# Performance work log

Hardware: AMD Instinct MI355X
Metric: run time of the kernel (lower is better)

## Reference

```python
import jax, jax.numpy as jnp
import numpy as np

EPS_NORM = 1e-12   # torch F.normalize eps
GN_EPS = 1e-5      # GroupNorm eps
FACTOR = 5
NUM_HEADS = 8
NEG_SLOPE = 0.01   # LeakyReLU default


def _l2norm(x, axis):
    n = jnp.sqrt(jnp.sum(x * x, axis=axis, keepdims=True))
    return x / jnp.maximum(n, EPS_NORM)


def setup_inputs() -> dict:
    key = jax.random.key(0)
    B, C, H, W, D = 2, 256, 16, 16, 16
    N = H * W * D
    sample_k = FACTOR * int(np.ceil(np.log(N)))  # 45
    ks = jax.random.split(key, 8)
    s = 0.02
    return {
        "x": jax.random.normal(ks[0], (B, C, H, W, D), jnp.float32),
        "W_qkvv": jax.random.normal(ks[1], (C, 4 * C), jnp.float32) * s,
        "W_out": jax.random.normal(ks[2], (C, C), jnp.float32) * s,
        "b_out": jnp.zeros((C,), jnp.float32),
        "W_out2": jax.random.normal(ks[3], (C, C), jnp.float32) * s,
        "b_out2": jnp.zeros((C,), jnp.float32),
        "gamma1": 0.1 * jnp.ones((C,), jnp.float32),
        "conv_w": jax.random.normal(ks[4], (C, C, 3, 3, 3), jnp.float32) * s,
        "gn_w": jnp.ones((C,), jnp.float32),
        "gn_b": jnp.zeros((C,), jnp.float32),
        "index_sample": jax.random.randint(ks[5], (N, sample_k), 0, N),
    }


def reference(x, W_qkvv, W_out, b_out, W_out2, b_out2, gamma1, conv_w, gn_w, gn_b, index_sample):
    B, C, H, Wd, D = x.shape
    N = H * Wd * D
    nh = NUM_HEADS
    dh = C // nh
    xs = x.reshape(B, C, N).transpose(0, 2, 1)                    # [B,N,C]
    qkvv = (xs @ W_qkvv).reshape(B, N, 4, nh, dh).transpose(2, 0, 3, 1, 4)  # [4,B,nh,N,dh]
    q, k, v_ca, v_sa = qkvv[0], qkvv[1], qkvv[2], qkvv[3]
    q = _l2norm(q, axis=-2)   # normalize over sequence dim (dim=-2 in torch)
    k = _l2norm(k, axis=-2)

    u = FACTOR * int(np.ceil(np.log(N)))
    # --- ProbSparse _prob_QK ---
    K_sample = k[:, :, index_sample, :]                            # [B,nh,N,sk,dh]
    QK_sample = jnp.einsum('bhle,bhlse->bhls', q, K_sample)        # [B,nh,N,sk]
    M = QK_sample.max(-1) - QK_sample.sum(-1) / N                  # sparsity measure
    _, M_top = jax.lax.top_k(M, u)                                 # [B,nh,u]
    b_idx = jnp.arange(B)[:, None, None]
    h_idx = jnp.arange(nh)[None, :, None]
    Q_red = q[b_idx, h_idx, M_top]                                 # [B,nh,u,dh]
    scores = jnp.einsum('bhud,bhld->bhul', Q_red, k)               # [B,nh,u,N]

    # --- spatial (ProbSparse) context ---
    ctx = jnp.broadcast_to(v_sa.mean(axis=-2, keepdims=True), v_sa.shape)  # [B,nh,N,dh]
    attn_sa = jax.nn.softmax(scores, axis=-1)
    upd = jnp.einsum('bhul,bhld->bhud', attn_sa, v_sa)             # [B,nh,u,dh]
    ctx = ctx.at[b_idx, h_idx, M_top].set(upd)

    # --- channel attention (on transposed q,k,v: [B,nh,dh,N]) ---
    qt = q.transpose(0, 1, 3, 2)
    kt = k.transpose(0, 1, 3, 2)
    vt = v_ca.transpose(0, 1, 3, 2)
    attn_ca = jax.nn.softmax(jnp.einsum('bhdn,bhen->bhde', qt, kt), axis=-1)  # [B,nh,dh,dh]
    x_ca = jnp.einsum('bhde,bhen->bhdn', attn_ca, vt).transpose(0, 3, 1, 2).reshape(B, N, C)
    x_sa = ctx.transpose(0, 3, 1, 2).reshape(B, N, C)              # matches source permute
    x_sa = x_sa @ W_out + b_out                                    # dead branch (source discards)
    x_ca = x_ca @ W_out2 + b_out2
    epa = x_ca  # source: x = x_SA + x_CA; x = x_CA  -> only CA branch survives

    attn = xs + gamma1 * epa                                       # [B,N,C]
    attn = attn.reshape(B, H, Wd, D, C).transpose(0, 4, 1, 2, 3)   # [B,C,H,W,D]

    # conv8: Dropout3d (eval=id) -> Conv3d(3x3x3, no bias) -> GroupNorm(1 group)
    y = jax.lax.conv_general_dilated(attn, conv_w, (1, 1, 1), [(1, 1)] * 3,
                                     dimension_numbers=('NCDHW', 'OIDHW', 'NCDHW'))
    mu = y.mean(axis=(1, 2, 3, 4), keepdims=True)
    var = y.var(axis=(1, 2, 3, 4), keepdims=True)
    y = (y - mu) / jnp.sqrt(var + GN_EPS)
    y = y * gn_w[None, :, None, None, None] + gn_b[None, :, None, None, None]
    y = y + attn
    return jnp.where(y >= 0, y, NEG_SLOPE * y)
```

## Files before the change

### kernel.cpp

```cpp
#include <hip/hip_runtime.h>
#include <hip/hip_bf16.h>
#include <stdint.h>


#define B_ 2
#define C_ 256
#define N_ 4096
#define NH 8
#define PADV 5832
#define CN  (C_*N_)
#define BCN (B_*CN)

typedef unsigned short u16;
typedef unsigned int   u32;

using frag16 = __attribute__((ext_vector_type(8))) short;
using f32x4  = __attribute__((ext_vector_type(4))) float;

__device__ __forceinline__ u16 f2bf(float f) {
    u32 u = __float_as_uint(f);
    u += 0x7fff + ((u >> 16) & 1);
    return (u16)(u >> 16);
}
__device__ __forceinline__ float bb(u16 h) { return __uint_as_float((u32)h << 16); }
__device__ __forceinline__ void gld16(const void* g, void* l) {
    __builtin_amdgcn_global_load_lds((const __attribute__((address_space(1))) u32*)g,
                                     (__attribute__((address_space(3))) u32*)l, 16, 0, 0);
}
__device__ __forceinline__ int padrow(int n) {
    int z = n >> 8, y = (n >> 4) & 15, x = n & 15;
    return (z + 1) * 324 + (y + 1) * 18 + (x + 1);
}

#define OFF_XB16  0
#define OFF_GP    1048576
#define OFF_NQK   2097152
#define OFF_PK    0
#define OFF_Y     3145728
#define OFF_ATTB  4194304
#define OFF_ATTP  5242880
#define OFF_WT2   6735872
#define OFF_W2B   7620608
#define OFF_WQB   7653376
#define OFF_XT    7751680
#define OFF_WVT   8800256
#define OFF_BD    8833024
#define OFF_MT    8898560
#define OFF_WFU   8964096
#define OFF_NRM   9029632
#define OFF_RED   9030656

__global__ __launch_bounds__(256) void k_prep(const float* __restrict__ CW, const float* __restrict__ W2,
                                              const float* __restrict__ Wq, const float* __restrict__ X,
                                              u16* __restrict__ WT2, u16* __restrict__ W2B,
                                              u16* __restrict__ Wqb, u16* __restrict__ WvT,
                                              u16* __restrict__ XT, u16* __restrict__ XB,
                                              u32* __restrict__ APz, float* __restrict__ NRM) {
    __shared__ __align__(16) float ls[6912];
    float (*ts)[33] = (float(*)[33])ls;
    float (*t64)[65] = (float(*)[65])ls;
    int blk = blockIdx.x, tid = threadIdx.x;
    if (blk < 256) {
        int co = blk;
        const float* src = CW + (size_t)co * 6912;
        for (int u = tid; u < 6912; u += 256) ls[u] = src[u];
        __syncthreads();
#pragma unroll
        for (int t = 0; t < 27; ++t)
            WT2[(((size_t)t * 256 + co) << 8) + tid] = f2bf(ls[tid * 27 + t]);
    } else if (blk < 320) {
        int bi = blk - 256; int c0 = (bi & 7) * 32, p0 = (bi >> 3) * 32;
        int tx = tid & 31, ty = tid >> 5;
#pragma unroll
        for (int i = 0; i < 4; ++i) ts[ty + i * 8][tx] = W2[(size_t)(p0 + ty + i * 8) * 256 + c0 + tx];
        __syncthreads();
#pragma unroll
        for (int i = 0; i < 4; ++i) W2B[(size_t)(c0 + ty + i * 8) * 256 + p0 + tx] = f2bf(ts[tx][ty + i * 8]);
    } else if (blk < 512) {
        int bi = blk - 320; int c0 = (bi & 7) * 32, j0 = (bi >> 3) * 32;
        int tx = tid & 31, ty = tid >> 5;
#pragma unroll
        for (int i = 0; i < 4; ++i) ts[ty + i * 8][tx] = Wq[(size_t)(c0 + ty + i * 8) * 1024 + j0 + tx];
        __syncthreads();
#pragma unroll
        for (int i = 0; i < 4; ++i) Wqb[(size_t)(j0 + ty + i * 8) * 256 + c0 + tx] = f2bf(ts[tx][ty + i * 8]);
    } else if (blk < 768) {
        int c = blk - 512;
        WvT[(size_t)c * 256 + tid] = f2bf(Wq[(size_t)c * 1024 + 512 + tid]);
    } else if (blk < 1280) {
        int idx = blk - 768;
        int n0 = (idx & 63) * 64, c0 = ((idx >> 6) & 3) * 64, b = idx >> 8;
        int tn = tid & 63, tc4 = tid >> 6;
        const float* Xb = X + (size_t)b * CN;
        u16* XBb = XB + (size_t)b * CN;
#pragma unroll
        for (int i = 0; i < 16; ++i) {
            int c = c0 + tc4 + i * 4;
            float v = Xb[(size_t)c * N_ + n0 + tn];
            t64[tc4 + i * 4][tn] = v;
            XBb[(size_t)c * N_ + n0 + tn] = f2bf(v);
        }
        __syncthreads();
        u16* Xo = XT + (size_t)b * N_ * C_;
#pragma unroll
        for (int i = 0; i < 16; ++i)
            Xo[(size_t)(n0 + tc4 + i * 4) * C_ + c0 + tn] = f2bf(t64[tn][tc4 + i * 4]);
    } else if (blk < 7112) {
        APz[(size_t)(blk - 1280) * 256 + tid] = 0;
    } else {
        ((float4*)NRM)[tid] = make_float4(0.f, 0.f, 0.f, 0.f);
    }
}

__global__ __launch_bounds__(256) void k_gram(const u16* __restrict__ XB, float* __restrict__ GP) {
    __shared__ __align__(16) u16 As[2][8192], Bs[2][8192];
    int mt = blockIdx.x & 1, nt = blockIdx.x >> 1, s = blockIdx.y, b = blockIdx.z;
    int c0 = mt * 128, c0p = nt * 128, k0 = s * 512;
    int tid = threadIdx.x, lane = tid & 63, w = tid >> 6;
    int wm = w & 1, wn = w >> 1, qm = lane >> 4, lm = lane & 15;
    int srow = lane >> 3;
    int sperm = (((lane & 7) ^ srow) << 3);
    const u16* aB = XB + ((size_t)(b * 256 + c0 + w * 32 + srow)) * 4096 + k0 + sperm;
    const u16* bB = XB + ((size_t)(b * 256 + c0p + w * 32 + srow)) * 4096 + k0 + sperm;
    int rdp = ((lm & 7) << 3);
    f32x4 acc[4][4] = {};
    auto stg = [&](int p, int kt) {
#pragma unroll
        for (int i = 0; i < 4; ++i) {
            gld16(aB + (size_t)i * 32768 + kt * 64, &As[p][w * 2048 + i * 512]);
            gld16(bB + (size_t)i * 32768 + kt * 64, &Bs[p][w * 2048 + i * 512]);
        }
    };
    stg(0, 0);
#pragma unroll
    for (int kt = 0; kt < 8; ++kt) {
        int p = kt & 1;
        __syncthreads();
        if (kt < 7) stg(p ^ 1, kt + 1);
#pragma unroll
        for (int c2 = 0; c2 < 2; ++c2) {
            frag16 af[4], bf[4];
#pragma unroll
            for (int i = 0; i < 4; ++i)
                af[i] = *(const frag16*)&As[p][(wm * 64 + i * 16 + lm) * 64 + ((((c2 * 4 + qm) << 3) ^ rdp))];
#pragma unroll
            for (int j = 0; j < 4; ++j)
                bf[j] = *(const frag16*)&Bs[p][(wn * 64 + j * 16 + lm) * 64 + ((((c2 * 4 + qm) << 3) ^ rdp))];
#pragma unroll
            for (int i = 0; i < 4; ++i)
#pragma unroll
                for (int j = 0; j < 4; ++j)
                    acc[i][j] = __builtin_amdgcn_mfma_f32_16x16x32_bf16(af[i], bf[j], acc[i][j], 0, 0, 0);
        }
    }
    float* o = GP + (((size_t)s * B_ + b) * 256 + c0 + wm * 64) * 256 + c0p + wn * 64;
#pragma unroll
    for (int i = 0; i < 4; ++i)
#pragma unroll
        for (int j = 0; j < 4; ++j)
#pragma unroll
            for (int r = 0; r < 4; ++r)
                o[(size_t)(i * 16 + qm * 4 + r) * 256 + j * 16 + lm] = acc[i][j][r];
}

__global__ __launch_bounds__(256) void k_nqk(const float* __restrict__ GP, const u16* __restrict__ Wqb,
                                             u16* __restrict__ NQK, float* __restrict__ NRM) {
    __shared__ float Gs[16][260];
    int ct = blockIdx.x, h = blockIdx.y, b = blockIdx.z, t = threadIdx.x;
#pragma unroll
    for (int i = 0; i < 16; ++i) {
        float v = 0.f;
#pragma unroll
        for (int s = 0; s < 8; ++s)
            v += GP[(((size_t)s * B_ + b) * 256 + ct * 16 + i) * 256 + t];
        Gs[i][t] = v;
    }
    __syncthreads();
    int o = t >> 3, cg = t & 7;
    int cl0 = cg * 2, cl1 = cg * 2 + 1;
    const u16* Wk = Wqb + (size_t)(256 + h * 32 + o) * 256;
    const u16* Wqr = Wqb + (size_t)(h * 32 + o) * 256;
    float ak0 = 0.f, ak1 = 0.f, aq0 = 0.f, aq1 = 0.f;
    for (int cp = 0; cp < 256; cp += 8) {
        uint4 kv = *(const uint4*)(Wk + cp);
        uint4 qv = *(const uint4*)(Wqr + cp);
        const u16 *kh = (const u16*)&kv, *qh = (const u16*)&qv;
#pragma unroll
        for (int j = 0; j < 8; ++j) {
            float kf = bb(kh[j]), qf = bb(qh[j]);
            float g0 = Gs[cl0][cp + j], g1v = Gs[cl1][cp + j];
            ak0 += kf * g0; ak1 += kf * g1v;
            aq0 += qf * g0; aq1 += qf * g1v;
        }
    }
    size_t base_q = (((size_t)(b * NH + h) * 2 + 0) * 32 + o) * 256 + ct * 16 + cg * 2;
    *(u32*)(NQK + base_q)        = (u32)f2bf(aq0) | ((u32)f2bf(aq1) << 16);
    *(u32*)(NQK + base_q + 8192) = (u32)f2bf(ak0) | ((u32)f2bf(ak1) << 16);
    u32 wq = *(const u32*)(Wqr + ct * 16 + cg * 2);
    u32 wk = *(const u32*)(Wk + ct * 16 + cg * 2);
    float pq = bb((u16)wq) * aq0 + bb((u16)(wq >> 16)) * aq1;
    float pk = bb((u16)wk) * ak0 + bb((u16)(wk >> 16)) * ak1;
    pq += __shfl_xor(pq, 1); pq += __shfl_xor(pq, 2); pq += __shfl_xor(pq, 4);
    pk += __shfl_xor(pk, 1); pk += __shfl_xor(pk, 2); pk += __shfl_xor(pk, 4);
    if (cg == 0) {
        atomicAdd(&NRM[b * 512 + h * 64 + o], pq);
        atomicAdd(&NRM[b * 512 + h * 64 + 32 + o], pk);
    }
}

__global__ __launch_bounds__(256) void k_soft(const u16* __restrict__ NQK, const u16* __restrict__ Wqb,
                                              const float* __restrict__ NRM, u16* __restrict__ BD) {
    __shared__ __align__(16) u16 Ws[8192], Ns[8192];
    __shared__ float Sm[32][33];
    __shared__ float Ab[32][33];
    __shared__ float iqS[32], ikS[32];
    int h = blockIdx.x, b = blockIdx.y;
    int tid = threadIdx.x, lane = tid & 63, w = tid >> 6;
    int wm = w & 1, wn = w >> 1, qm = lane >> 4, lm = lane & 15;
    const u16* Wq = Wqb + ((size_t)h * 32) * 256;
    const u16* NK = NQK + (((size_t)(b * NH + h) * 2 + 1) * 32) * 256;
#pragma unroll
    for (int rp = 0; rp < 4; ++rp) {
        int row = rp * 8 + w * 2 + (lane >> 5);
        int cg = (lane & 31) ^ (row & 31);
        gld16(Wq + (size_t)row * 256 + cg * 8, &Ws[rp * 2048 + w * 512]);
        gld16(NK + (size_t)row * 256 + cg * 8, &Ns[rp * 2048 + w * 512]);
    }
    if (tid < 32) {
        iqS[tid] = 1.0f / fmaxf(sqrtf(fmaxf(NRM[b * 512 + h * 64 + tid], 0.f)), 1e-12f);
        ikS[tid] = 1.0f / fmaxf(sqrtf(fmaxf(NRM[b * 512 + h * 64 + 32 + tid], 0.f)), 1e-12f);
    }
    __syncthreads();
    f32x4 acc = {};
    int rowA = wm * 16 + lm, rowB = wn * 16 + lm;
#pragma unroll
    for (int kk = 0; kk < 8; ++kk) {
        int sA = ((kk * 4 + qm) ^ (rowA & 31)) << 3;
        int sB = ((kk * 4 + qm) ^ (rowB & 31)) << 3;
        frag16 af = *(const frag16*)&Ws[rowA * 256 + sA];
        frag16 bf = *(const frag16*)&Ns[rowB * 256 + sB];
        acc = __builtin_amdgcn_mfma_f32_16x16x32_bf16(af, bf, acc, 0, 0, 0);
    }
#pragma unroll
    for (int r = 0; r < 4; ++r) Sm[wm * 16 + qm * 4 + r][wn * 16 + lm] = acc[r];
    __syncthreads();
    if (tid < 32) {
        float iq = iqS[tid];
        float sv[32], m = -1e30f;
#pragma unroll
        for (int e = 0; e < 32; ++e) { sv[e] = Sm[tid][e] * iq * ikS[e]; m = fmaxf(m, sv[e]); }
        float sm = 0.f;
#pragma unroll
        for (int e = 0; e < 32; ++e) { sv[e] = __expf(sv[e] - m); sm += sv[e]; }
        float rin = 1.0f / sm;
#pragma unroll
        for (int e = 0; e < 32; ++e) Ab[tid][e] = sv[e] * rin;
    }
    __syncthreads();
    u16* Bo = BD + ((size_t)b * 256 + h * 32) * 256 + tid;
    bool own = (tid >> 5) == h;
    int e = tid & 31;
#pragma unroll
    for (int d = 0; d < 32; ++d)
        Bo[(size_t)d * 256] = own ? f2bf(Ab[d][e]) : (u16)0;
}

__global__ __launch_bounds__(256) void k_mt(const u16* __restrict__ WvT, const u16* __restrict__ BD,
                                            u16* __restrict__ MT) {
    __shared__ __align__(16) u16 As[2][8192], Bs[2][8192];
    int c0 = blockIdx.x * 128, j0 = blockIdx.y * 128, b = blockIdx.z;
    int tid = threadIdx.x, lane = tid & 63, w = tid >> 6;
    int wm = w & 1, wn = w >> 1, qm = lane >> 4, lm = lane & 15;
    int srow = lane >> 3;
    int sperm = (((lane & 7) ^ srow) << 3);
    const u16* aB = WvT + ((size_t)(c0 + w * 32 + srow)) * 256 + sperm;
    const u16* bB = BD + ((size_t)(b * 256 + j0 + w * 32 + srow)) * 256 + sperm;
    int rdp = ((lm & 7) << 3);
    f32x4 acc[4][4] = {};
    auto stg = [&](int p, int kc) {
#pragma unroll
        for (int i = 0; i < 4; ++i) {
            gld16(aB + i * 2048 + kc * 64, &As[p][w * 2048 + i * 512]);
            gld16(bB + i * 2048 + kc * 64, &Bs[p][w * 2048 + i * 512]);
        }
    };
    stg(0, 0);
#pragma unroll
    for (int kt = 0; kt < 4; ++kt) {
        int p = kt & 1;
        __syncthreads();
        if (kt < 3) stg(p ^ 1, kt + 1);
#pragma unroll
        for (int c2 = 0; c2 < 2; ++c2) {
            frag16 af[4], bf[4];
#pragma unroll
            for (int i = 0; i < 4; ++i)
                af[i] = *(const frag16*)&As[p][(wm * 64 + i * 16 + lm) * 64 + ((((c2 * 4 + qm) << 3) ^ rdp))];
#pragma unroll
            for (int j = 0; j < 4; ++j)
                bf[j] = *(const frag16*)&Bs[p][(wn * 64 + j * 16 + lm) * 64 + ((((c2 * 4 + qm) << 3) ^ rdp))];
#pragma unroll
            for (int i = 0; i < 4; ++i)
#pragma unroll
                for (int j = 0; j < 4; ++j)
                    acc[i][j] = __builtin_amdgcn_mfma_f32_16x16x32_bf16(af[i], bf[j], acc[i][j], 0, 0, 0);
        }
    }
#pragma unroll
    for (int i = 0; i < 4; ++i)
#pragma unroll
        for (int r = 0; r < 4; ++r) {
            int c = c0 + wm * 64 + i * 16 + qm * 4 + r;
#pragma unroll
            for (int j = 0; j < 4; ++j)
                MT[((size_t)b * 256 + c) * 256 + j0 + wn * 64 + j * 16 + lm] = f2bf(acc[i][j][r]);
        }
}

__global__ __launch_bounds__(256) void k_wfull(const u16* __restrict__ W2B, const u16* __restrict__ MT,
                                               const float* __restrict__ g1, u16* __restrict__ WFU) {
    __shared__ __align__(16) u16 As[2][8192], Bs[2][8192];
    int c0 = blockIdx.x * 128, cq0 = blockIdx.y * 128, b = blockIdx.z;
    int tid = threadIdx.x, lane = tid & 63, w = tid >> 6;
    int wm = w & 1, wn = w >> 1, qm = lane >> 4, lm = lane & 15;
    int srow = lane >> 3;
    int sperm = (((lane & 7) ^ srow) << 3);
    const u16* aB = W2B + ((size_t)(c0 + w * 32 + srow)) * 256 + sperm;
    const u16* bB = MT + ((size_t)(b * 256 + cq0 + w * 32 + srow)) * 256 + sperm;
    int rdp = ((lm & 7) << 3);
    f32x4 acc[4][4] = {};
    auto stg = [&](int p, int kc) {
#pragma unroll
        for (int i = 0; i < 4; ++i) {
            gld16(aB + i * 2048 + kc * 64, &As[p][w * 2048 + i * 512]);
            gld16(bB + i * 2048 + kc * 64, &Bs[p][w * 2048 + i * 512]);
        }
    };
    stg(0, 0);
#pragma unroll
    for (int kt = 0; kt < 4; ++kt) {
        int p = kt & 1;
        __syncthreads();
        if (kt < 3) stg(p ^ 1, kt + 1);
#pragma unroll
        for (int c2 = 0; c2 < 2; ++c2) {
            frag16 af[4], bf[4];
#pragma unroll
            for (int i = 0; i < 4; ++i)
                af[i] = *(const frag16*)&As[p][(wm * 64 + i * 16 + lm) * 64 + ((((c2 * 4 + qm) << 3) ^ rdp))];
#pragma unroll
            for (int j = 0; j < 4; ++j)
                bf[j] = *(const frag16*)&Bs[p][(wn * 64 + j * 16 + lm) * 64 + ((((c2 * 4 + qm) << 3) ^ rdp))];
#pragma unroll
            for (int i = 0; i < 4; ++i)
#pragma unroll
                for (int j = 0; j < 4; ++j)
                    acc[i][j] = __builtin_amdgcn_mfma_f32_16x16x32_bf16(af[i], bf[j], acc[i][j], 0, 0, 0);
        }
    }
#pragma unroll
    for (int i = 0; i < 4; ++i)
#pragma unroll
        for (int r = 0; r < 4; ++r) {
            int c = c0 + wm * 64 + i * 16 + qm * 4 + r;
            float gv = g1[c];
#pragma unroll
            for (int j = 0; j < 4; ++j) {
                int cc = cq0 + wn * 64 + j * 16 + lm;
                WFU[((size_t)b * 256 + c) * 256 + cc] = f2bf(gv * acc[i][j][r]);
            }
        }
}

__global__ __launch_bounds__(256) void k_att(const u16* __restrict__ WFU, const u16* __restrict__ XT,
                                             const float* __restrict__ bias2, const float* __restrict__ g1,
                                             const float* __restrict__ X, u16* __restrict__ ATTb,
                                             u16* __restrict__ ATTp) {
    __shared__ __align__(16) u16 As[2][8192], Bs[2][8192];
    int n0 = blockIdx.x * 128, c0 = blockIdx.y * 128, b = blockIdx.z;
    int tid = threadIdx.x, lane = tid & 63, w = tid >> 6;
    int wm = w & 1, wn = w >> 1, qm = lane >> 4, lm = lane & 15;
    int srow = lane >> 3;
    int sperm = (((lane & 7) ^ srow) << 3);
    const u16* aB = WFU + ((size_t)(b * 256 + c0 + w * 32 + srow)) * 256 + sperm;
    const u16* bB = XT + ((size_t)(b * N_ + n0 + w * 32 + srow)) * 256 + sperm;
    int rdp = ((lm & 7) << 3);
    f32x4 acc[4][4] = {};
    auto stg = [&](int p, int kc) {
#pragma unroll
        for (int i = 0; i < 4; ++i) {
            gld16(aB + i * 2048 + kc * 64, &As[p][w * 2048 + i * 512]);
            gld16(bB + i * 2048 + kc * 64, &Bs[p][w * 2048 + i * 512]);
        }
    };
    stg(0, 0);
#pragma unroll
    for (int kt = 0; kt < 4; ++kt) {
        int p = kt & 1;
        __syncthreads();
        if (kt < 3) stg(p ^ 1, kt + 1);
#pragma unroll
        for (int c2 = 0; c2 < 2; ++c2) {
            frag16 af[4], bf[4];
#pragma unroll
            for (int i = 0; i < 4; ++i)
                af[i] = *(const frag16*)&As[p][(wm * 64 + i * 16 + lm) * 64 + ((((c2 * 4 + qm) << 3) ^ rdp))];
#pragma unroll
            for (int j = 0; j < 4; ++j)
                bf[j] = *(const frag16*)&Bs[p][(wn * 64 + j * 16 + lm) * 64 + ((((c2 * 4 + qm) << 3) ^ rdp))];
#pragma unroll
            for (int i = 0; i < 4; ++i)
#pragma unroll
                for (int j = 0; j < 4; ++j)
                    acc[i][j] = __builtin_amdgcn_mfma_f32_16x16x32_bf16(af[i], bf[j], acc[i][j], 0, 0, 0);
        }
    }
    int c_base = c0 + wm * 64, n_base = n0 + wn * 64;
    const float* xin = X + (size_t)b * CN;
    u16* Ao = ATTb + (size_t)b * CN;
    u16* Ap = ATTp + ((size_t)b * PADV << 8);
    float val[4][4][4];
#pragma unroll
    for (int i = 0; i < 4; ++i)
#pragma unroll
        for (int r = 0; r < 4; ++r) {
            int c = c_base + i * 16 + qm * 4 + r;
            float gb2 = g1[c] * bias2[c];
#pragma unroll
            for (int j = 0; j < 4; ++j) {
                int n = n_base + j * 16 + lm;
                float v = xin[(size_t)c * N_ + n] + acc[i][j][r] + gb2;
                val[i][j][r] = v;
                Ao[(size_t)c * N_ + n] = f2bf(v);
            }
        }
#pragma unroll
    for (int j = 0; j < 4; ++j) {
        int n = n_base + j * 16 + lm;
        int pr = padrow(n);
#pragma unroll
        for (int i = 0; i < 4; ++i) {
            ushort4 pk;
            pk.x = f2bf(val[i][j][0]); pk.y = f2bf(val[i][j][1]);
            pk.z = f2bf(val[i][j][2]); pk.w = f2bf(val[i][j][3]);
            *(ushort4*)&Ap[((size_t)pr << 8) + c_base + i * 16 + qm * 4] = pk;
        }
    }
}

__global__ __launch_bounds__(256) void k_conv_mfma(const u16* __restrict__ WT2, const u16* __restrict__ ATTp,
                                                   u16* __restrict__ Pk) {
    __shared__ __align__(16) u16 As[2][8192], Bs[2][8192];
    int n0 = blockIdx.x * 128;
    int co0 = (blockIdx.y & 1) * 128, ks = blockIdx.y >> 1;
    int b = blockIdx.z;
    int tid = threadIdx.x, lane = tid & 63, w = tid >> 6;
    int wm = w & 1, wn = w >> 1, qm = lane >> 4, lm = lane & 15;
    int srow = lane >> 3;
    int sperm = (((lane & 7) ^ srow) << 3);
    const u16* aB = WT2 + (((size_t)ks * 9 * 256 + co0 + w * 32 + srow) << 8) + sperm;
    int prA[4];
#pragma unroll
    for (int i = 0; i < 4; ++i) prA[i] = padrow(n0 + w * 32 + i * 8 + srow) << 8;
    const u16* bB = ATTp + ((size_t)b * PADV << 8) + ((ks - 1) * 324 << 8) + sperm;
    int rdp = ((lm & 7) << 3);
    f32x4 acc[4][4] = {};
    auto stg = [&](int p, int kt) {
        int tap9 = kt >> 2, kc = kt & 3;
        int K9 = ((tap9 / 3) - 1) * 18 + (tap9 % 3 - 1);
#pragma unroll
        for (int i = 0; i < 4; ++i) {
            gld16(aB + (size_t)tap9 * 65536 + i * 2048 + kc * 64, &As[p][w * 2048 + i * 512]);
            gld16(bB + prA[i] + K9 * 256 + kc * 64,              &Bs[p][w * 2048 + i * 512]);
        }
    };
    stg(0, 0);
#pragma unroll
    for (int kt = 0; kt < 36; ++kt) {
        int p = kt & 1;
        __syncthreads();
        if (kt < 35) stg(p ^ 1, kt + 1);
#pragma unroll
        for (int c2 = 0; c2 < 2; ++c2) {
            frag16 af[4], bf[4];
#pragma unroll
            for (int i = 0; i < 4; ++i)
                af[i] = *(const frag16*)&As[p][(wm * 64 + i * 16 + lm) * 64 + ((((c2 * 4 + qm) << 3) ^ rdp))];
#pragma unroll
            for (int j = 0; j < 4; ++j)
                bf[j] = *(const frag16*)&Bs[p][(wn * 64 + j * 16 + lm) * 64 + ((((c2 * 4 + qm) << 3) ^ rdp))];
#pragma unroll
            for (int i = 0; i < 4; ++i)
#pragma unroll
                for (int j = 0; j < 4; ++j)
                    acc[i][j] = __builtin_amdgcn_mfma_f32_16x16x32_bf16(af[i], bf[j], acc[i][j], 0, 0, 0);
        }
    }
    u16* Pb = Pk + ((size_t)(ks * B_ + b) * C_ + co0 + wm * 64) * N_ + n0 + wn * 64;
#pragma unroll
    for (int i = 0; i < 4; ++i)
#pragma unroll
        for (int j = 0; j < 4; ++j)
#pragma unroll
            for (int r = 0; r < 4; ++r)
                Pb[(size_t)(i * 16 + qm * 4 + r) * N_ + j * 16 + lm] = f2bf(acc[i][j][r]);
}

__global__ __launch_bounds__(256) void k_gn_reduce(const u16* __restrict__ Pk, u16* __restrict__ Y,
                                                   float* __restrict__ RED) {
    int blk = blockIdx.x, b = blockIdx.y;
    size_t base = (size_t)b * CN + (size_t)blk * 16384;
    const u16* p0 = Pk + base;
    const u16* p1 = Pk + BCN + base;
    const u16* p2 = Pk + (size_t)2 * BCN + base;
    u16* y = Y + base;
    float s = 0.f, q = 0.f;
    for (int u = threadIdx.x * 8; u < 16384; u += 2048) {
        uint4 a = *(const uint4*)&p0[u];
        uint4 c1 = *(const uint4*)&p1[u];
        uint4 c2 = *(const uint4*)&p2[u];
        const u16 *A = (const u16*)&a, *B1 = (const u16*)&c1, *C2 = (const u16*)&c2;
        __align__(16) u16 outp[8];
#pragma unroll
        for (int i = 0; i < 8; ++i) {
            float v = bb(A[i]) + bb(B1[i]) + bb(C2[i]);
            s += v; q += v * v;
            outp[i] = f2bf(v);
        }
        *(uint4*)&y[u] = *(const uint4*)outp;
    }
#pragma unroll
    for (int off = 32; off; off >>= 1) { s += __shfl_down(s, off); q += __shfl_down(q, off); }
    __shared__ float rs_[4], rq[4];
    int lane = threadIdx.x & 63, wv = threadIdx.x >> 6;
    if (!lane) { rs_[wv] = s; rq[wv] = q; }
    __syncthreads();
    if (threadIdx.x == 0) {
        RED[((size_t)b * 64 + blk) * 2 + 0] = rs_[0] + rs_[1] + rs_[2] + rs_[3];
        RED[((size_t)b * 64 + blk) * 2 + 1] = rq[0] + rq[1] + rq[2] + rq[3];
    }
}

__global__ __launch_bounds__(256) void k_final(const u16* __restrict__ Y, const u16* __restrict__ ATTb,
                                               const float* __restrict__ RED, const float* __restrict__ gw,
                                               const float* __restrict__ gb, float* __restrict__ out) {
    int i = blockIdx.x * 256 + threadIdx.x;
    int b = i >> 20;
    int c = (i >> 12) & 255;
    __shared__ float smu[2];
    if (threadIdx.x < 64) {
        float s = RED[((size_t)b * 64 + threadIdx.x) * 2 + 0];
        float q = RED[((size_t)b * 64 + threadIdx.x) * 2 + 1];
#pragma unroll
        for (int off = 32; off; off >>= 1) { s += __shfl_down(s, off); q += __shfl_down(q, off); }
        if (threadIdx.x == 0) {
            float inv = 1.0f / (float)CN;
            float mu = s * inv, var = q * inv - mu * mu;
            smu[0] = mu; smu[1] = rsqrtf(var + 1e-5f);
        }
    }
    __syncthreads();
    float v = (bb(Y[i]) - smu[0]) * smu[1] * gw[c] + gb[c] + bb(ATTb[i]);
    out[i] = v >= 0.f ? v : 0.01f * v;
}

extern "C" void kernel_launch(void* const* d_in, const int* in_sizes, int n_in,
                              void* d_out, int out_size, void* d_ws, size_t ws_size,
                              hipStream_t stream) {
    const float* x      = (const float*)d_in[0];
    const float* Wqkvv  = (const float*)d_in[1];
    const float* W_out2 = (const float*)d_in[4];
    const float* b_out2 = (const float*)d_in[5];
    const float* gamma1 = (const float*)d_in[6];
    const float* conv_w = (const float*)d_in[7];
    const float* gn_w   = (const float*)d_in[8];
    const float* gn_b   = (const float*)d_in[9];
    float* out = (float*)d_out;
    float* ws = (float*)d_ws;

    u16*   XB   = (u16*)(ws + OFF_XB16);
    float* GP   = ws + OFF_GP;
    u16*   NQK  = (u16*)(ws + OFF_NQK);
    u16*   Pk   = (u16*)(ws + OFF_PK);
    u16*   Y    = (u16*)(ws + OFF_Y);
    u16*   ATTb = (u16*)(ws + OFF_ATTB);
    u16*   ATTp = (u16*)(ws + OFF_ATTP);
    u16*   WT2  = (u16*)(ws + OFF_WT2);
    u16*   W2B  = (u16*)(ws + OFF_W2B);
    u16*   Wqb  = (u16*)(ws + OFF_WQB);
    u16*   XT   = (u16*)(ws + OFF_XT);
    u16*   WvT  = (u16*)(ws + OFF_WVT);
    u16*   BD   = (u16*)(ws + OFF_BD);
    u16*   MT   = (u16*)(ws + OFF_MT);
    u16*   WFU  = (u16*)(ws + OFF_WFU);
    float* NRM  = ws + OFF_NRM;
    float* RED  = ws + OFF_RED;

    k_prep      <<<7113, 256, 0, stream>>>(conv_w, W_out2, Wqkvv, x, WT2, W2B, Wqb, WvT, XT, XB, (u32*)ATTp, NRM);
    k_gram      <<<dim3(4, 8, B_), 256, 0, stream>>>(XB, GP);
    k_nqk       <<<dim3(16, NH, B_), 256, 0, stream>>>(GP, Wqb, NQK, NRM);
    k_soft      <<<dim3(NH, B_), 256, 0, stream>>>(NQK, Wqb, NRM, BD);
    k_mt        <<<dim3(2, 2, B_), 256, 0, stream>>>(WvT, BD, MT);
    k_wfull     <<<dim3(2, 2, B_), 256, 0, stream>>>(W2B, MT, gamma1, WFU);
    k_att       <<<dim3(32, 2, B_), 256, 0, stream>>>(WFU, XT, b_out2, gamma1, x, ATTb, ATTp);
    k_conv_mfma <<<dim3(32, 6, B_), 256, 0, stream>>>(WT2, ATTp, Pk);
    k_gn_reduce <<<dim3(64, B_), 256, 0, stream>>>(Pk, Y, RED);
    k_final     <<<8192, 256, 0, stream>>>(Y, ATTb, RED, gn_w, gn_b, out);
}
```

Before: 198.5 us.

## Fuse block-diagonal MT product into softmax kernel and halve conv N-tile

The softmax kernel now multiplies its per-head 32x32 attention block directly with the matching WvT slice using MFMA and writes MT. This removes the dense block-diagonal BD buffer and the separate k_mt GEMM launch, which mostly multiplied zeros. Separately, the conv MFMA kernel's N tile drops from 128 to 64, doubling the grid to 768 blocks so more of the machine is occupied, at the cost of less reuse of the weight tile per block.

```diff
diff --git a/kernel.cpp b/kernel.cpp
--- a/kernel.cpp
+++ b/kernel.cpp
@@ -44,7 +44,6 @@
 #define OFF_WQB   7653376
 #define OFF_XT    7751680
 #define OFF_WVT   8800256
-#define OFF_BD    8833024
 #define OFF_MT    8898560
 #define OFF_WFU   8964096
 #define OFF_NRM   9029632
@@ -209,7 +208,8 @@
 }
 
 __global__ __launch_bounds__(256) void k_soft(const u16* __restrict__ NQK, const u16* __restrict__ Wqb,
-                                              const float* __restrict__ NRM, u16* __restrict__ BD) {
+                                              const u16* __restrict__ WvT, const float* __restrict__ NRM,
+                                              u16* __restrict__ MT) {
     __shared__ __align__(16) u16 Ws[8192], Ns[8192];
     __shared__ float Sm[32][33];
     __shared__ float Ab[32][33];
@@ -257,64 +257,31 @@
         for (int e = 0; e < 32; ++e) Ab[tid][e] = sv[e] * rin;
     }
     __syncthreads();
-    u16* Bo = BD + ((size_t)b * 256 + h * 32) * 256 + tid;
-    bool own = (tid >> 5) == h;
-    int e = tid & 31;
-#pragma unroll
-    for (int d = 0; d < 32; ++d)
-        Bo[(size_t)d * 256] = own ? f2bf(Ab[d][e]) : (u16)0;
-}
-
-__global__ __launch_bounds__(256) void k_mt(const u16* __restrict__ WvT, const u16* __restrict__ BD,
-                                            u16* __restrict__ MT) {
-    __shared__ __align__(16) u16 As[2][8192], Bs[2][8192];
-    int c0 = blockIdx.x * 128, j0 = blockIdx.y * 128, b = blockIdx.z;
-    int tid = threadIdx.x, lane = tid & 63, w = tid >> 6;
-    int wm = w & 1, wn = w >> 1, qm = lane >> 4, lm = lane & 15;
-    int srow = lane >> 3;
-    int sperm = (((lane & 7) ^ srow) << 3);
-    const u16* aB = WvT + ((size_t)(c0 + w * 32 + srow)) * 256 + sperm;
-    const u16* bB = BD + ((size_t)(b * 256 + j0 + w * 32 + srow)) * 256 + sperm;
-    int rdp = ((lm & 7) << 3);
-    f32x4 acc[4][4] = {};
-    auto stg = [&](int p, int kc) {
-#pragma unroll
-        for (int i = 0; i < 4; ++i) {
-            gld16(aB + i * 2048 + kc * 64, &As[p][w * 2048 + i * 512]);
-            gld16(bB + i * 2048 + kc * 64, &Bs[p][w * 2048 + i * 512]);
-        }
-    };
-    stg(0, 0);
-#pragma unroll
-    for (int kt = 0; kt < 4; ++kt) {
-        int p = kt & 1;
-        __syncthreads();
-        if (kt < 3) stg(p ^ 1, kt + 1);
-#pragma unroll
-        for (int c2 = 0; c2 < 2; ++c2) {
-            frag16 af[4], bf[4];
-#pragma unroll
-            for (int i = 0; i < 4; ++i)
-                af[i] = *(const frag16*)&As[p][(wm * 64 + i * 16 + lm) * 64 + ((((c2 * 4 + qm) << 3) ^ rdp))];
-#pragma unroll
-            for (int j = 0; j < 4; ++j)
-                bf[j] = *(const frag16*)&Bs[p][(wn * 64 + j * 16 + lm) * 64 + ((((c2 * 4 + qm) << 3) ^ rdp))];
-#pragma unroll
-            for (int i = 0; i < 4; ++i)
-#pragma unroll
-                for (int j = 0; j < 4; ++j)
-                    acc[i][j] = __builtin_amdgcn_mfma_f32_16x16x32_bf16(af[i], bf[j], acc[i][j], 0, 0, 0);
-        }
-    }
+    frag16 bf2[2];
+#pragma unroll
+    for (int j = 0; j < 2; ++j) {
+        __align__(16) u16 tmp[8];
+#pragma unroll
+        for (int ii = 0; ii < 8; ++ii) tmp[ii] = f2bf(Ab[j * 16 + lm][qm * 8 + ii]);
+        bf2[j] = *(const frag16*)tmp;
+    }
+    f32x4 acc2[4][2] = {};
+#pragma unroll
+    for (int i = 0; i < 4; ++i) {
+        int row = w * 64 + i * 16 + lm;
+        frag16 af = *(const frag16*)&WvT[(size_t)row * 256 + h * 32 + qm * 8];
+#pragma unroll
+        for (int j = 0; j < 2; ++j)
+            acc2[i][j] = __builtin_amdgcn_mfma_f32_16x16x32_bf16(af, bf2[j], acc2[i][j], 0, 0, 0);
+    }
+    u16* Mo = MT + (size_t)b * 65536;
 #pragma unroll
     for (int i = 0; i < 4; ++i)
 #pragma unroll
-        for (int r = 0; r < 4; ++r) {
-            int c = c0 + wm * 64 + i * 16 + qm * 4 + r;
-#pragma unroll
-            for (int j = 0; j < 4; ++j)
-                MT[((size_t)b * 256 + c) * 256 + j0 + wn * 64 + j * 16 + lm] = f2bf(acc[i][j][r]);
-        }
+        for (int j = 0; j < 2; ++j)
+#pragma unroll
+            for (int r = 0; r < 4; ++r)
+                Mo[(size_t)(w * 64 + i * 16 + qm * 4 + r) * 256 + h * 32 + j * 16 + lm] = f2bf(acc2[i][j][r]);
 }
 
 __global__ __launch_bounds__(256) void k_wfull(const u16* __restrict__ W2B, const u16* __restrict__ MT,
@@ -450,8 +417,8 @@
 
 __global__ __launch_bounds__(256) void k_conv_mfma(const u16* __restrict__ WT2, const u16* __restrict__ ATTp,
                                                    u16* __restrict__ Pk) {
-    __shared__ __align__(16) u16 As[2][8192], Bs[2][8192];
-    int n0 = blockIdx.x * 128;
+    __shared__ __align__(16) u16 As[2][8192], Bs[2][4096];
+    int n0 = blockIdx.x * 64;
     int co0 = (blockIdx.y & 1) * 128, ks = blockIdx.y >> 1;
     int b = blockIdx.z;
     int tid = threadIdx.x, lane = tid & 63, w = tid >> 6;
@@ -459,20 +426,21 @@
     int srow = lane >> 3;
     int sperm = (((lane & 7) ^ srow) << 3);
     const u16* aB = WT2 + (((size_t)ks * 9 * 256 + co0 + w * 32 + srow) << 8) + sperm;
-    int prA[4];
-#pragma unroll
-    for (int i = 0; i < 4; ++i) prA[i] = padrow(n0 + w * 32 + i * 8 + srow) << 8;
+    int prA[2];
+#pragma unroll
+    for (int i = 0; i < 2; ++i) prA[i] = padrow(n0 + w * 16 + i * 8 + srow) << 8;
     const u16* bB = ATTp + ((size_t)b * PADV << 8) + ((ks - 1) * 324 << 8) + sperm;
     int rdp = ((lm & 7) << 3);
-    f32x4 acc[4][4] = {};
+    f32x4 acc[4][2] = {};
     auto stg = [&](int p, int kt) {
         int tap9 = kt >> 2, kc = kt & 3;
         int K9 = ((tap9 / 3) - 1) * 18 + (tap9 % 3 - 1);
 #pragma unroll
-        for (int i = 0; i < 4; ++i) {
+        for (int i = 0; i < 4; ++i)
             gld16(aB + (size_t)tap9 * 65536 + i * 2048 + kc * 64, &As[p][w * 2048 + i * 512]);
-            gld16(bB + prA[i] + K9 * 256 + kc * 64,              &Bs[p][w * 2048 + i * 512]);
-        }
+#pragma unroll
+        for (int i = 0; i < 2; ++i)
+            gld16(bB + prA[i] + K9 * 256 + kc * 64, &Bs[p][w * 1024 + i * 512]);
     };
     stg(0, 0);
 #pragma unroll
@@ -482,25 +450,25 @@
         if (kt < 35) stg(p ^ 1, kt + 1);
 #pragma unroll
         for (int c2 = 0; c2 < 2; ++c2) {
-            frag16 af[4], bf[4];
+            frag16 af[4], bf[2];
 #pragma unroll
             for (int i = 0; i < 4; ++i)
                 af[i] = *(const frag16*)&As[p][(wm * 64 + i * 16 + lm) * 64 + ((((c2 * 4 + qm) << 3) ^ rdp))];
 #pragma unroll
-            for (int j = 0; j < 4; ++j)
-                bf[j] = *(const frag16*)&Bs[p][(wn * 64 + j * 16 + lm) * 64 + ((((c2 * 4 + qm) << 3) ^ rdp))];
-#pragma unroll
-            for (int i = 0; i < 4; ++i)
-#pragma unroll
-                for (int j = 0; j < 4; ++j)
+            for (int j = 0; j < 2; ++j)
+                bf[j] = *(const frag16*)&Bs[p][(wn * 32 + j * 16 + lm) * 64 + ((((c2 * 4 + qm) << 3) ^ rdp))];
+#pragma unroll
+            for (int i = 0; i < 4; ++i)
+#pragma unroll
+                for (int j = 0; j < 2; ++j)
                     acc[i][j] = __builtin_amdgcn_mfma_f32_16x16x32_bf16(af[i], bf[j], acc[i][j], 0, 0, 0);
         }
     }
-    u16* Pb = Pk + ((size_t)(ks * B_ + b) * C_ + co0 + wm * 64) * N_ + n0 + wn * 64;
+    u16* Pb = Pk + ((size_t)(ks * B_ + b) * C_ + co0 + wm * 64) * N_ + n0 + wn * 32;
 #pragma unroll
     for (int i = 0; i < 4; ++i)
 #pragma unroll
-        for (int j = 0; j < 4; ++j)
+        for (int j = 0; j < 2; ++j)
 #pragma unroll
             for (int r = 0; r < 4; ++r)
                 Pb[(size_t)(i * 16 + qm * 4 + r) * N_ + j * 16 + lm] = f2bf(acc[i][j][r]);
@@ -590,7 +558,6 @@
     u16*   Wqb  = (u16*)(ws + OFF_WQB);
     u16*   XT   = (u16*)(ws + OFF_XT);
     u16*   WvT  = (u16*)(ws + OFF_WVT);
-    u16*   BD   = (u16*)(ws + OFF_BD);
     u16*   MT   = (u16*)(ws + OFF_MT);
     u16*   WFU  = (u16*)(ws + OFF_WFU);
     float* NRM  = ws + OFF_NRM;
@@ -599,11 +566,10 @@
     k_prep      <<<7113, 256, 0, stream>>>(conv_w, W_out2, Wqkvv, x, WT2, W2B, Wqb, WvT, XT, XB, (u32*)ATTp, NRM);
     k_gram      <<<dim3(4, 8, B_), 256, 0, stream>>>(XB, GP);
     k_nqk       <<<dim3(16, NH, B_), 256, 0, stream>>>(GP, Wqb, NQK, NRM);
-    k_soft      <<<dim3(NH, B_), 256, 0, stream>>>(NQK, Wqb, NRM, BD);
-    k_mt        <<<dim3(2, 2, B_), 256, 0, stream>>>(WvT, BD, MT);
+    k_soft      <<<dim3(NH, B_), 256, 0, stream>>>(NQK, Wqb, WvT, NRM, MT);
     k_wfull     <<<dim3(2, 2, B_), 256, 0, stream>>>(W2B, MT, gamma1, WFU);
     k_att       <<<dim3(32, 2, B_), 256, 0, stream>>>(WFU, XT, b_out2, gamma1, x, ATTb, ATTp);
-    k_conv_mfma <<<dim3(32, 6, B_), 256, 0, stream>>>(WT2, ATTp, Pk);
+    k_conv_mfma <<<dim3(64, 6, B_), 256, 0, stream>>>(WT2, ATTp, Pk);
     k_gn_reduce <<<dim3(64, B_), 256, 0, stream>>>(Pk, Y, RED);
     k_final     <<<8192, 256, 0, stream>>>(Y, ATTb, RED, gn_w, gn_b, out);
 }
```

After: 182.4 us. 1.09x faster.
